# Kernel tuning notes

Measured on AMD Instinct MI355X. Metric: run time of the kernel, lower is better.

The kernel has to match this reference:

```python
import jax, jax.numpy as jnp
import numpy as np

N, E, H, C = 50000, 800000, 4, 32   # nodes, edges, heads, per-head channels
HID, LAT, G = H * C, 32, 128        # hidden, latent, num graphs
IN_DIM = 64
NEG_SLOPE = 0.2
BN_EPS = 1e-5


def setup_inputs() -> dict:
    key = jax.random.key(0)
    ks = jax.random.split(key, 20)
    inp = {
        "x": jax.random.normal(ks[0], (N, IN_DIM), jnp.float32),
        "edge_index": jax.random.randint(ks[1], (2, E), 0, N, jnp.int32),
        "batch": jnp.sort(jax.random.randint(ks[2], (N,), 0, G, jnp.int32)),
        # layer 0
        "W0": jax.random.normal(ks[3], (IN_DIM, HID), jnp.float32) * (1.0 / np.sqrt(IN_DIM)),
        "a_src0": jax.random.normal(ks[4], (H, C), jnp.float32) * 0.1,
        "a_dst0": jax.random.normal(ks[5], (H, C), jnp.float32) * 0.1,
        "b0": jnp.zeros((HID,), jnp.float32),
        # layer 1
        "W1": jax.random.normal(ks[6], (HID, HID), jnp.float32) * (1.0 / np.sqrt(HID)),
        "a_src1": jax.random.normal(ks[7], (H, C), jnp.float32) * 0.1,
        "a_dst1": jax.random.normal(ks[8], (H, C), jnp.float32) * 0.1,
        "b1": jnp.zeros((HID,), jnp.float32),
        # layer 2
        "W2": jax.random.normal(ks[9], (HID, HID), jnp.float32) * (1.0 / np.sqrt(HID)),
        "a_src2": jax.random.normal(ks[10], (H, C), jnp.float32) * 0.1,
        "a_dst2": jax.random.normal(ks[11], (H, C), jnp.float32) * 0.1,
        "b2": jnp.zeros((HID,), jnp.float32),
        # head
        "fc_w": jax.random.normal(ks[12], (HID, LAT), jnp.float32) * (1.0 / np.sqrt(HID)),
        "fc_b": jnp.zeros((LAT,), jnp.float32),
        "bn_g": jnp.ones((LAT,), jnp.float32),
        "bn_b": jnp.zeros((LAT,), jnp.float32),
    }
    return inp


def _gat_conv(x, src, dst, W, a_src, a_dst, b):
    n = x.shape[0]
    h = (x @ W).reshape(n, H, C)                      # [N,H,C]
    alpha_s = jnp.einsum("nhc,hc->nh", h, a_src)       # [N,H]
    alpha_d = jnp.einsum("nhc,hc->nh", h, a_dst)
    e = jax.nn.leaky_relu(alpha_s[src] + alpha_d[dst], NEG_SLOPE)  # [E',H]
    # scatter-softmax over incoming edges of each dst node
    m = jax.ops.segment_max(e, dst, num_segments=n)
    m = jnp.where(jnp.isfinite(m), m, 0.0)
    ex = jnp.exp(e - m[dst])
    denom = jax.ops.segment_sum(ex, dst, num_segments=n)
    alpha = ex / (denom[dst] + 1e-16)                  # [E',H]
    out = jax.ops.segment_sum(alpha[:, :, None] * h[src], dst, num_segments=n)
    return out.reshape(n, H * C) + b


def reference(x, edge_index, batch, W0, a_src0, a_dst0, b0, W1, a_src1, a_dst1, b1,
              W2, a_src2, a_dst2, b2, fc_w, fc_b, bn_g, bn_b):
    # PyG GATConv default add_self_loops=True
    loop = jnp.arange(N, dtype=edge_index.dtype)
    src = jnp.concatenate([edge_index[0], loop])
    dst = jnp.concatenate([edge_index[1], loop])

    h = x
    for (W, a_s, a_d, b) in ((W0, a_src0, a_dst0, b0),
                             (W1, a_src1, a_dst1, b1),
                             (W2, a_src2, a_dst2, b2)):
        h = _gat_conv(h, src, dst, W, a_s, a_d, b)
        h = jax.nn.leaky_relu(h, NEG_SLOPE)  # dropout is identity in eval

    pooled = jax.ops.segment_sum(h, batch, num_segments=G)  # global_add_pool -> [G,HID]
    out = pooled @ fc_w + fc_b
    # BatchNorm1d in eval mode with running_mean=0, running_var=1
    out = bn_g * out * (1.0 / np.sqrt(1.0 + BN_EPS)) + bn_b
    return out
```

## Files before the change

### kernel.cpp

```cpp
#include <hip/hip_runtime.h>
#include <hip/hip_bf16.h>
#include <float.h>

#define NEG 0.2f

__device__ __forceinline__ float leaky(float x) { return x > 0.0f ? x : NEG * x; }

__device__ __forceinline__ unsigned short f2bf(float f) {
  unsigned x = __float_as_uint(f);
  unsigned r = (x + 0x7fffu + ((x >> 16) & 1u)) >> 16;
  return (unsigned short)r;
}

__device__ __forceinline__ float2 bf2f2(unsigned u) {
  float2 r;
  r.x = __uint_as_float(u << 16);
  r.y = __uint_as_float(u & 0xffff0000u);
  return r;
}

__global__ void zero_kernel(int* __restrict__ p, int n) {
  int i = blockIdx.x * blockDim.x + threadIdx.x;
  int stride = gridDim.x * blockDim.x;
  for (; i < n; i += stride) p[i] = 0;
}

__global__ void count_kernel(const int* __restrict__ ei, int* __restrict__ deg, int E, int N) {
  int i = blockIdx.x * blockDim.x + threadIdx.x;
  if (i >= E + N) return;
  int dst = (i < E) ? ei[E + i] : (i - E);
  atomicAdd(&deg[dst], 1);
}

__global__ __launch_bounds__(1024) void scan_block_kernel(const int* __restrict__ deg,
                                                          int* __restrict__ row_start,
                                                          int* __restrict__ sums, int n) {
  __shared__ int buf[1024];
  int t = threadIdx.x;
  int idx = blockIdx.x * 1024 + t;
  int x = (idx < n) ? deg[idx] : 0;
  int v = x;
  buf[t] = v;
  __syncthreads();
  for (int off = 1; off < 1024; off <<= 1) {
    int a = (t >= off) ? buf[t - off] : 0;
    __syncthreads();
    v += a;
    buf[t] = v;
    __syncthreads();
  }
  if (idx < n) row_start[idx] = v - x;
  if (t == 1023) sums[blockIdx.x] = v;
}

__global__ __launch_bounds__(1024) void scan_sums_kernel(int* __restrict__ sums,
                                                         int* __restrict__ row_start,
                                                         int nch, int n) {
  __shared__ int buf[1024];
  int t = threadIdx.x;
  int x = (t < nch) ? sums[t] : 0;
  int v = x;
  buf[t] = v;
  __syncthreads();
  for (int off = 1; off < 1024; off <<= 1) {
    int a = (t >= off) ? buf[t - off] : 0;
    __syncthreads();
    v += a;
    buf[t] = v;
    __syncthreads();
  }
  if (t < nch) sums[t] = v - x;
  if (t == 1023) row_start[n] = v;
}

__global__ __launch_bounds__(1024) void scan_add_kernel(int* __restrict__ row_start,
                                                        const int* __restrict__ sums, int n) {
  int idx = blockIdx.x * 1024 + threadIdx.x;
  if (idx < n) row_start[idx] += sums[blockIdx.x];
}

__global__ void fill_kernel(const int* __restrict__ ei, int* __restrict__ cursor,
                            const int* __restrict__ row_start, int* __restrict__ csr_src,
                            int E, int N) {
  int i = blockIdx.x * blockDim.x + threadIdx.x;
  if (i >= E + N) return;
  int src, dst;
  if (i < E) { src = ei[i]; dst = ei[E + i]; } else { src = dst = i - E; }
  int pos = atomicAdd(&cursor[dst], 1);
  csr_src[row_start[dst] + pos] = src;
}

__global__ __launch_bounds__(256) void gemm_kernel(const float* __restrict__ X,
                                                   const float* __restrict__ W,
                                                   unsigned short* __restrict__ Hb,
                                                   const float* __restrict__ a_src,
                                                   const float* __restrict__ a_dst,
                                                   float* __restrict__ as_arr,
                                                   float* __restrict__ ad_arr,
                                                   int nrows, int K) {
  __shared__ float Xs[64][36];
  __shared__ float Ws[32][132];
  int t = threadIdx.x;
  int row0 = blockIdx.x * 64;
  int tcol = t & 31;
  int trow = t >> 5;
  float acc[8][4];
#pragma unroll
  for (int i = 0; i < 8; ++i)
#pragma unroll
    for (int j = 0; j < 4; ++j) acc[i][j] = 0.0f;

  for (int kb = 0; kb < K; kb += 32) {
#pragma unroll
    for (int p = 0; p < 2; ++p) {
      int flat = t + p * 256;
      int r = flat >> 3;
      int kq = (flat & 7) * 4;
      float4 v = make_float4(0.f, 0.f, 0.f, 0.f);
      int gr = row0 + r;
      if (gr < nrows) v = *(const float4*)(X + (size_t)gr * K + kb + kq);
      *(float4*)(&Xs[r][kq]) = v;
    }
#pragma unroll
    for (int p = 0; p < 4; ++p) {
      int flat = t + p * 256;
      int r = flat >> 5;
      int cq = (flat & 31) * 4;
      float4 v = *(const float4*)(W + (size_t)(kb + r) * 128 + cq);
      *(float4*)(&Ws[r][cq]) = v;
    }
    __syncthreads();
#pragma unroll
    for (int kk = 0; kk < 32; kk += 4) {
      float4 xv[8];
#pragma unroll
      for (int i = 0; i < 8; ++i) xv[i] = *(const float4*)(&Xs[trow + 8 * i][kk]);
#pragma unroll
      for (int q = 0; q < 4; ++q) {
        float4 wv = *(const float4*)(&Ws[kk + q][tcol * 4]);
#pragma unroll
        for (int i = 0; i < 8; ++i) {
          float xq = (q == 0) ? xv[i].x : (q == 1) ? xv[i].y : (q == 2) ? xv[i].z : xv[i].w;
          acc[i][0] += xq * wv.x;
          acc[i][1] += xq * wv.y;
          acc[i][2] += xq * wv.z;
          acc[i][3] += xq * wv.w;
        }
      }
    }
    __syncthreads();
  }

  float4 as4 = *(const float4*)(a_src + tcol * 4);
  float4 ad4 = *(const float4*)(a_dst + tcol * 4);
  float ps[8], pd[8];
#pragma unroll
  for (int i = 0; i < 8; ++i) {
    int r = row0 + trow + 8 * i;
    if (r < nrows) {
      union { unsigned short u[4]; uint2 v; } pk;
      pk.u[0] = f2bf(acc[i][0]);
      pk.u[1] = f2bf(acc[i][1]);
      pk.u[2] = f2bf(acc[i][2]);
      pk.u[3] = f2bf(acc[i][3]);
      *(uint2*)(Hb + (size_t)r * 128 + tcol * 4) = pk.v;
    }
    ps[i] = acc[i][0] * as4.x + acc[i][1] * as4.y + acc[i][2] * as4.z + acc[i][3] * as4.w;
    pd[i] = acc[i][0] * ad4.x + acc[i][1] * ad4.y + acc[i][2] * ad4.z + acc[i][3] * ad4.w;
  }
#pragma unroll
  for (int off = 1; off < 8; off <<= 1) {
#pragma unroll
    for (int i = 0; i < 8; ++i) {
      ps[i] += __shfl_xor(ps[i], off);
      pd[i] += __shfl_xor(pd[i], off);
    }
  }
  if ((tcol & 7) == 0) {
    int head = tcol >> 3;
#pragma unroll
    for (int i = 0; i < 8; ++i) {
      int r = row0 + trow + 8 * i;
      if (r < nrows) {
        as_arr[(size_t)r * 4 + head] = ps[i];
        ad_arr[(size_t)r * 4 + head] = pd[i];
      }
    }
  }
}

template <int POOL>
__global__ __launch_bounds__(256) void agg_kernel(const unsigned short* __restrict__ Hb,
                                                  const float* __restrict__ as_arr,
                                                  const float* __restrict__ ad_arr,
                                                  const int* __restrict__ csr_src,
                                                  const int* __restrict__ row_start,
                                                  const float* __restrict__ bias,
                                                  float* __restrict__ xnext,
                                                  const int* __restrict__ batch,
                                                  float* __restrict__ pooled, int N) {
  int wid = threadIdx.x >> 6;
  int lane = threadIdx.x & 63;
  int n = blockIdx.x * 4 + wid;
  if (n >= N) return;
  int rs = row_start[n], re = row_start[n + 1];
  int head = lane >> 4;
  float ad_h = ad_arr[(size_t)n * 4 + head];

  const unsigned* hp = (const unsigned*)Hb + lane;
  float denom = 0.f, acc0 = 0.f, acc1 = 0.f;
  int i = rs;
  for (; i + 2 <= re; i += 2) {
    int s0 = csr_src[i], s1 = csr_src[i + 1];
    float a0 = as_arr[(size_t)s0 * 4 + head];
    float a1 = as_arr[(size_t)s1 * 4 + head];
    unsigned u0 = hp[(size_t)s0 * 64];
    unsigned u1 = hp[(size_t)s1 * 64];
    float e0 = __expf(fminf(leaky(a0 + ad_h), 80.f));
    float e1 = __expf(fminf(leaky(a1 + ad_h), 80.f));
    float2 h0 = bf2f2(u0);
    float2 h1 = bf2f2(u1);
    denom += e0 + e1;
    acc0 += e0 * h0.x + e1 * h1.x;
    acc1 += e0 * h0.y + e1 * h1.y;
  }
  if (i < re) {
    int s0 = csr_src[i];
    float a0 = as_arr[(size_t)s0 * 4 + head];
    unsigned u0 = hp[(size_t)s0 * 64];
    float e0 = __expf(fminf(leaky(a0 + ad_h), 80.f));
    float2 h0 = bf2f2(u0);
    denom += e0;
    acc0 += e0 * h0.x;
    acc1 += e0 * h0.y;
  }
  float inv = 1.0f / (denom + 1e-16f);
  float2 bv = *(const float2*)(bias + 2 * lane);
  float v0 = leaky(acc0 * inv + bv.x);
  float v1 = leaky(acc1 * inv + bv.y);
  if (POOL) {
    int g = batch[n];
    atomicAdd(&pooled[(size_t)g * 128 + 2 * lane], v0);
    atomicAdd(&pooled[(size_t)g * 128 + 2 * lane + 1], v1);
  } else {
    *(float2*)(xnext + (size_t)n * 128 + 2 * lane) = make_float2(v0, v1);
  }
}

__global__ void head_kernel(const float* __restrict__ pooled, const float* __restrict__ fc_w,
                            const float* __restrict__ fc_b, const float* __restrict__ bn_g,
                            const float* __restrict__ bn_b, float* __restrict__ out, int G) {
  int t = threadIdx.x;
  int g = blockIdx.x * 8 + (t >> 5);
  int j = t & 31;
  if (g >= G) return;
  const float* pr = pooled + (size_t)g * 128;
  float acc = 0.f;
#pragma unroll 8
  for (int k = 0; k < 128; ++k) acc += pr[k] * fc_w[k * 32 + j];
  const float inv = 0.9999950000374997f;
  out[g * 32 + j] = bn_g[j] * (acc + fc_b[j]) * inv + bn_b[j];
}

extern "C" void kernel_launch(void* const* d_in, const int* in_sizes, int n_in,
                              void* d_out, int out_size, void* d_ws, size_t ws_size,
                              hipStream_t stream) {
  const float* x = (const float*)d_in[0];
  const int* ei = (const int*)d_in[1];
  const int* batch = (const int*)d_in[2];
  const float* Wm[3] = {(const float*)d_in[3], (const float*)d_in[7], (const float*)d_in[11]};
  const float* a_s[3] = {(const float*)d_in[4], (const float*)d_in[8], (const float*)d_in[12]};
  const float* a_d[3] = {(const float*)d_in[5], (const float*)d_in[9], (const float*)d_in[13]};
  const float* bb[3] = {(const float*)d_in[6], (const float*)d_in[10], (const float*)d_in[14]};
  const float* fc_w = (const float*)d_in[15];
  const float* fc_b = (const float*)d_in[16];
  const float* bn_g = (const float*)d_in[17];
  const float* bn_b = (const float*)d_in[18];
  float* out = (float*)d_out;

  int N = in_sizes[0] / 64;
  int E = in_sizes[1] / 2;
  int G = out_size / 32;
  int Etot = E + N;

  char* p = (char*)d_ws;
  auto carve = [&](size_t bytes) {
    char* r = p;
    p += (bytes + 255) & ~size_t(255);
    return r;
  };
  int* deg       = (int*)carve((size_t)N * 4);
  int* cursor    = (int*)carve((size_t)N * 4);
  float* pooled  = (float*)carve((size_t)G * 128 * 4);
  int* row_start = (int*)carve((size_t)(N + 1) * 4);
  int* sums      = (int*)carve(4096);
  int* csr_src   = (int*)carve((size_t)Etot * 4);
  unsigned short* Hb = (unsigned short*)carve((size_t)N * 128 * 2);
  float* bufX    = (float*)carve((size_t)N * 128 * 4);
  float* as_arr  = (float*)carve((size_t)N * 4 * 4);
  float* ad_arr  = (float*)carve((size_t)N * 4 * 4);

  int nz = (int)(((char*)(pooled + (size_t)G * 128) - (char*)deg) / 4);
  zero_kernel<<<512, 256, 0, stream>>>(deg, nz);

  int egrid = (Etot + 255) / 256;
  count_kernel<<<egrid, 256, 0, stream>>>(ei, deg, E, N);
  int nch = (N + 1023) / 1024;
  scan_block_kernel<<<nch, 1024, 0, stream>>>(deg, row_start, sums, N);
  scan_sums_kernel<<<1, 1024, 0, stream>>>(sums, row_start, nch, N);
  scan_add_kernel<<<nch, 1024, 0, stream>>>(row_start, sums, N);
  fill_kernel<<<egrid, 256, 0, stream>>>(ei, cursor, row_start, csr_src, E, N);

  int ggrid = (N + 63) / 64;
  int ngrid = (N + 3) / 4;

  gemm_kernel<<<ggrid, 256, 0, stream>>>(x, Wm[0], Hb, a_s[0], a_d[0], as_arr, ad_arr, N, 64);
  agg_kernel<0><<<ngrid, 256, 0, stream>>>(Hb, as_arr, ad_arr, csr_src, row_start, bb[0],
                                           bufX, nullptr, nullptr, N);
  gemm_kernel<<<ggrid, 256, 0, stream>>>(bufX, Wm[1], Hb, a_s[1], a_d[1], as_arr, ad_arr, N, 128);
  agg_kernel<0><<<ngrid, 256, 0, stream>>>(Hb, as_arr, ad_arr, csr_src, row_start, bb[1],
                                           bufX, nullptr, nullptr, N);
  gemm_kernel<<<ggrid, 256, 0, stream>>>(bufX, Wm[2], Hb, a_s[2], a_d[2], as_arr, ad_arr, N, 128);
  agg_kernel<1><<<ngrid, 256, 0, stream>>>(Hb, as_arr, ad_arr, csr_src, row_start, bb[2],
                                           nullptr, batch, pooled, N);

  head_kernel<<<(G + 7) / 8, 256, 0, stream>>>(pooled, fc_w, fc_b, bn_g, bn_b, out, G);
}
```

Measured before the change: 514.3 us.

## Restructure GAT aggregation to cooperative edge-weight staging and 4-edge-parallel 16B gathers

The aggregation kernel now computes attention exponentials for up to 64 edges at once, one edge per lane and all four heads per edge, and stages them in shared memory together with the source indices. The wave then splits into four quarter-waves that each gather a different edge's full 256-byte bf16 row with 16-byte loads and accumulate 8 channels per lane. The partial sums are combined with cross-lane shuffles and written by one quarter-wave. This removes the redundant per-lane exp and attention loads and raises memory-level parallelism, at the cost of more registers, shared-memory traffic, a reduction step, and 48 idle lanes during the final write.

```diff
diff --git a/kernel.cpp b/kernel.cpp
--- a/kernel.cpp
+++ b/kernel.cpp
@@ -199,51 +199,86 @@
                                                   float* __restrict__ xnext,
                                                   const int* __restrict__ batch,
                                                   float* __restrict__ pooled, int N) {
+  __shared__ float eL[4][64][4];
+  __shared__ int iL[4][64];
   int wid = threadIdx.x >> 6;
   int lane = threadIdx.x & 63;
+  int q = lane >> 4;
+  int ql = lane & 15;
+  int h = ql >> 2;
   int n = blockIdx.x * 4 + wid;
   if (n >= N) return;
   int rs = row_start[n], re = row_start[n + 1];
-  int head = lane >> 4;
-  float ad_h = ad_arr[(size_t)n * 4 + head];
-
-  const unsigned* hp = (const unsigned*)Hb + lane;
-  float denom = 0.f, acc0 = 0.f, acc1 = 0.f;
-  int i = rs;
-  for (; i + 2 <= re; i += 2) {
-    int s0 = csr_src[i], s1 = csr_src[i + 1];
-    float a0 = as_arr[(size_t)s0 * 4 + head];
-    float a1 = as_arr[(size_t)s1 * 4 + head];
-    unsigned u0 = hp[(size_t)s0 * 64];
-    unsigned u1 = hp[(size_t)s1 * 64];
-    float e0 = __expf(fminf(leaky(a0 + ad_h), 80.f));
-    float e1 = __expf(fminf(leaky(a1 + ad_h), 80.f));
-    float2 h0 = bf2f2(u0);
-    float2 h1 = bf2f2(u1);
-    denom += e0 + e1;
-    acc0 += e0 * h0.x + e1 * h1.x;
-    acc1 += e0 * h0.y + e1 * h1.y;
-  }
-  if (i < re) {
-    int s0 = csr_src[i];
-    float a0 = as_arr[(size_t)s0 * 4 + head];
-    unsigned u0 = hp[(size_t)s0 * 64];
-    float e0 = __expf(fminf(leaky(a0 + ad_h), 80.f));
-    float2 h0 = bf2f2(u0);
-    denom += e0;
-    acc0 += e0 * h0.x;
-    acc1 += e0 * h0.y;
-  }
-  float inv = 1.0f / (denom + 1e-16f);
-  float2 bv = *(const float2*)(bias + 2 * lane);
-  float v0 = leaky(acc0 * inv + bv.x);
-  float v1 = leaky(acc1 * inv + bv.y);
-  if (POOL) {
-    int g = batch[n];
-    atomicAdd(&pooled[(size_t)g * 128 + 2 * lane], v0);
-    atomicAdd(&pooled[(size_t)g * 128 + 2 * lane + 1], v1);
-  } else {
-    *(float2*)(xnext + (size_t)n * 128 + 2 * lane) = make_float2(v0, v1);
+  int deg = re - rs;
+  float4 adn = *(const float4*)(ad_arr + (size_t)n * 4);
+
+  float acc[8];
+#pragma unroll
+  for (int j = 0; j < 8; ++j) acc[j] = 0.f;
+  float denom = 0.f;
+
+  for (int base = 0; base < deg; base += 64) {
+    int pos = rs + base + lane;
+    int idx = 0;
+    float4 e4 = make_float4(0.f, 0.f, 0.f, 0.f);
+    if (pos < re) {
+      idx = csr_src[pos];
+      float4 a4 = *(const float4*)(as_arr + (size_t)idx * 4);
+      e4.x = __expf(fminf(leaky(a4.x + adn.x), 80.f));
+      e4.y = __expf(fminf(leaky(a4.y + adn.y), 80.f));
+      e4.z = __expf(fminf(leaky(a4.z + adn.z), 80.f));
+      e4.w = __expf(fminf(leaky(a4.w + adn.w), 80.f));
+    }
+    iL[wid][lane] = idx;
+    *(float4*)(&eL[wid][lane][0]) = e4;
+
+    int nr = deg - base; if (nr > 64) nr = 64;
+    int rounds = (nr + 3) >> 2;
+    for (int r = 0; r < rounds; ++r) {
+      int sl = 4 * r + q;
+      float ex = eL[wid][sl][h];
+      int s = iL[wid][sl];
+      uint4 u = *(const uint4*)(Hb + ((size_t)s << 7) + (ql << 3));
+      float2 f;
+      f = bf2f2(u.x); acc[0] += ex * f.x; acc[1] += ex * f.y;
+      f = bf2f2(u.y); acc[2] += ex * f.x; acc[3] += ex * f.y;
+      f = bf2f2(u.z); acc[4] += ex * f.x; acc[5] += ex * f.y;
+      f = bf2f2(u.w); acc[6] += ex * f.x; acc[7] += ex * f.y;
+      denom += ex;
+    }
+  }
+
+#pragma unroll
+  for (int off = 16; off <= 32; off <<= 1) {
+#pragma unroll
+    for (int j = 0; j < 8; ++j) acc[j] += __shfl_xor(acc[j], off);
+    denom += __shfl_xor(denom, off);
+  }
+
+  if (q == 0) {
+    float inv = 1.0f / (denom + 1e-16f);
+    float4 b0 = *(const float4*)(bias + ql * 8);
+    float4 b1 = *(const float4*)(bias + ql * 8 + 4);
+    float v0 = leaky(acc[0] * inv + b0.x);
+    float v1 = leaky(acc[1] * inv + b0.y);
+    float v2 = leaky(acc[2] * inv + b0.z);
+    float v3 = leaky(acc[3] * inv + b0.w);
+    float v4 = leaky(acc[4] * inv + b1.x);
+    float v5 = leaky(acc[5] * inv + b1.y);
+    float v6 = leaky(acc[6] * inv + b1.z);
+    float v7 = leaky(acc[7] * inv + b1.w);
+    if (POOL) {
+      int g = batch[n];
+      float* pp = pooled + (size_t)g * 128 + ql * 8;
+      atomicAdd(pp + 0, v0); atomicAdd(pp + 1, v1);
+      atomicAdd(pp + 2, v2); atomicAdd(pp + 3, v3);
+      atomicAdd(pp + 4, v4); atomicAdd(pp + 5, v5);
+      atomicAdd(pp + 6, v6); atomicAdd(pp + 7, v7);
+    } else {
+      float* xp = xnext + (size_t)n * 128 + ql * 8;
+      *(float4*)(xp + 0) = make_float4(v0, v1, v2, v3);
+      *(float4*)(xp + 4) = make_float4(v4, v5, v6, v7);
+    }
   }
 }
 
```

New measurement: 749.9 us. 45.8% more time.

## Precompute per-edge attention exponentials in a separate edge kernel before aggregation

Applied to the files above, without the earlier changes.

Adds an edge-parallel kernel that computes exp(leaky(as[src]+ad[dst])) for all four heads per CSR edge and stores it in a new edge array, using a new csr_dst array written by fill. The aggregation kernel then reads the precomputed weights instead of gathering as_arr and evaluating exp in each of the 16 lanes per head, and its edge loop is unrolled from 2 to 4. This removes redundant exp work and scattered as_arr gathers from the aggregation, but adds an extra launch per layer and roughly 19 MB of extra edge-array traffic per layer.

```diff
diff --git a/kernel.cpp b/kernel.cpp
--- a/kernel.cpp
+++ b/kernel.cpp
@@ -81,13 +81,15 @@
 
 __global__ void fill_kernel(const int* __restrict__ ei, int* __restrict__ cursor,
                             const int* __restrict__ row_start, int* __restrict__ csr_src,
-                            int E, int N) {
+                            int* __restrict__ csr_dst, int E, int N) {
   int i = blockIdx.x * blockDim.x + threadIdx.x;
   if (i >= E + N) return;
   int src, dst;
   if (i < E) { src = ei[i]; dst = ei[E + i]; } else { src = dst = i - E; }
   int pos = atomicAdd(&cursor[dst], 1);
-  csr_src[row_start[dst] + pos] = src;
+  int slot = row_start[dst] + pos;
+  csr_src[slot] = src;
+  csr_dst[slot] = dst;
 }
 
 __global__ __launch_bounds__(256) void gemm_kernel(const float* __restrict__ X,
@@ -189,10 +191,28 @@
   }
 }
 
+__global__ __launch_bounds__(256) void ecomp_kernel(const int* __restrict__ csr_src,
+                                                    const int* __restrict__ csr_dst,
+                                                    const float* __restrict__ as_arr,
+                                                    const float* __restrict__ ad_arr,
+                                                    float* __restrict__ earr, int Etot) {
+  int i = blockIdx.x * 256 + threadIdx.x;
+  if (i >= Etot) return;
+  int s = csr_src[i];
+  int d = csr_dst[i];
+  float4 a = *(const float4*)(as_arr + (size_t)s * 4);
+  float4 b = *(const float4*)(ad_arr + (size_t)d * 4);
+  float4 e;
+  e.x = __expf(fminf(leaky(a.x + b.x), 80.f));
+  e.y = __expf(fminf(leaky(a.y + b.y), 80.f));
+  e.z = __expf(fminf(leaky(a.z + b.z), 80.f));
+  e.w = __expf(fminf(leaky(a.w + b.w), 80.f));
+  *(float4*)(earr + (size_t)i * 4) = e;
+}
+
 template <int POOL>
 __global__ __launch_bounds__(256) void agg_kernel(const unsigned short* __restrict__ Hb,
-                                                  const float* __restrict__ as_arr,
-                                                  const float* __restrict__ ad_arr,
+                                                  const float* __restrict__ earr,
                                                   const int* __restrict__ csr_src,
                                                   const int* __restrict__ row_start,
                                                   const float* __restrict__ bias,
@@ -205,34 +225,36 @@
   if (n >= N) return;
   int rs = row_start[n], re = row_start[n + 1];
   int head = lane >> 4;
-  float ad_h = ad_arr[(size_t)n * 4 + head];
 
   const unsigned* hp = (const unsigned*)Hb + lane;
+  const float* ep = earr + head;
   float denom = 0.f, acc0 = 0.f, acc1 = 0.f;
   int i = rs;
-  for (; i + 2 <= re; i += 2) {
-    int s0 = csr_src[i], s1 = csr_src[i + 1];
-    float a0 = as_arr[(size_t)s0 * 4 + head];
-    float a1 = as_arr[(size_t)s1 * 4 + head];
+  for (; i + 4 <= re; i += 4) {
+    int s0 = csr_src[i], s1 = csr_src[i + 1], s2 = csr_src[i + 2], s3 = csr_src[i + 3];
+    float e0 = ep[(size_t)i * 4];
+    float e1 = ep[(size_t)(i + 1) * 4];
+    float e2 = ep[(size_t)(i + 2) * 4];
+    float e3 = ep[(size_t)(i + 3) * 4];
     unsigned u0 = hp[(size_t)s0 * 64];
     unsigned u1 = hp[(size_t)s1 * 64];
-    float e0 = __expf(fminf(leaky(a0 + ad_h), 80.f));
-    float e1 = __expf(fminf(leaky(a1 + ad_h), 80.f));
-    float2 h0 = bf2f2(u0);
-    float2 h1 = bf2f2(u1);
-    denom += e0 + e1;
-    acc0 += e0 * h0.x + e1 * h1.x;
-    acc1 += e0 * h0.y + e1 * h1.y;
-  }
-  if (i < re) {
+    unsigned u2 = hp[(size_t)s2 * 64];
+    unsigned u3 = hp[(size_t)s3 * 64];
+    denom += (e0 + e1) + (e2 + e3);
+    float2 f;
+    f = bf2f2(u0); acc0 += e0 * f.x; acc1 += e0 * f.y;
+    f = bf2f2(u1); acc0 += e1 * f.x; acc1 += e1 * f.y;
+    f = bf2f2(u2); acc0 += e2 * f.x; acc1 += e2 * f.y;
+    f = bf2f2(u3); acc0 += e3 * f.x; acc1 += e3 * f.y;
+  }
+  for (; i < re; ++i) {
     int s0 = csr_src[i];
-    float a0 = as_arr[(size_t)s0 * 4 + head];
+    float e0 = ep[(size_t)i * 4];
     unsigned u0 = hp[(size_t)s0 * 64];
-    float e0 = __expf(fminf(leaky(a0 + ad_h), 80.f));
-    float2 h0 = bf2f2(u0);
+    float2 f = bf2f2(u0);
     denom += e0;
-    acc0 += e0 * h0.x;
-    acc1 += e0 * h0.y;
+    acc0 += e0 * f.x;
+    acc1 += e0 * f.y;
   }
   float inv = 1.0f / (denom + 1e-16f);
   float2 bv = *(const float2*)(bias + 2 * lane);
@@ -295,6 +317,8 @@
   int* row_start = (int*)carve((size_t)(N + 1) * 4);
   int* sums      = (int*)carve(4096);
   int* csr_src   = (int*)carve((size_t)Etot * 4);
+  int* csr_dst   = (int*)carve((size_t)Etot * 4);
+  float* earr    = (float*)carve((size_t)Etot * 4 * 4);
   unsigned short* Hb = (unsigned short*)carve((size_t)N * 128 * 2);
   float* bufX    = (float*)carve((size_t)N * 128 * 4);
   float* as_arr  = (float*)carve((size_t)N * 4 * 4);
@@ -309,19 +333,22 @@
   scan_block_kernel<<<nch, 1024, 0, stream>>>(deg, row_start, sums, N);
   scan_sums_kernel<<<1, 1024, 0, stream>>>(sums, row_start, nch, N);
   scan_add_kernel<<<nch, 1024, 0, stream>>>(row_start, sums, N);
-  fill_kernel<<<egrid, 256, 0, stream>>>(ei, cursor, row_start, csr_src, E, N);
+  fill_kernel<<<egrid, 256, 0, stream>>>(ei, cursor, row_start, csr_src, csr_dst, E, N);
 
   int ggrid = (N + 63) / 64;
   int ngrid = (N + 3) / 4;
 
   gemm_kernel<<<ggrid, 256, 0, stream>>>(x, Wm[0], Hb, a_s[0], a_d[0], as_arr, ad_arr, N, 64);
-  agg_kernel<0><<<ngrid, 256, 0, stream>>>(Hb, as_arr, ad_arr, csr_src, row_start, bb[0],
+  ecomp_kernel<<<egrid, 256, 0, stream>>>(csr_src, csr_dst, as_arr, ad_arr, earr, Etot);
+  agg_kernel<0><<<ngrid, 256, 0, stream>>>(Hb, earr, csr_src, row_start, bb[0],
                                            bufX, nullptr, nullptr, N);
   gemm_kernel<<<ggrid, 256, 0, stream>>>(bufX, Wm[1], Hb, a_s[1], a_d[1], as_arr, ad_arr, N, 128);
-  agg_kernel<0><<<ngrid, 256, 0, stream>>>(Hb, as_arr, ad_arr, csr_src, row_start, bb[1],
+  ecomp_kernel<<<egrid, 256, 0, stream>>>(csr_src, csr_dst, as_arr, ad_arr, earr, Etot);
+  agg_kernel<0><<<ngrid, 256, 0, stream>>>(Hb, earr, csr_src, row_start, bb[1],
                                            bufX, nullptr, nullptr, N);
   gemm_kernel<<<ggrid, 256, 0, stream>>>(bufX, Wm[2], Hb, a_s[2], a_d[2], as_arr, ad_arr, N, 128);
-  agg_kernel<1><<<ngrid, 256, 0, stream>>>(Hb, as_arr, ad_arr, csr_src, row_start, bb[2],
+  ecomp_kernel<<<egrid, 256, 0, stream>>>(csr_src, csr_dst, as_arr, ad_arr, earr, Etot);
+  agg_kernel<1><<<ngrid, 256, 0, stream>>>(Hb, earr, csr_src, row_start, bb[2],
                                            nullptr, batch, pooled, N);
 
   head_kernel<<<(G + 7) / 8, 256, 0, stream>>>(pooled, fc_w, fc_b, bn_g, bn_b, out, G);
```

Result: faster. 483.1 us (-6.1%).
